# Kernel optimization log

Hardware: AMD Instinct MI355X
Metric: run time of the kernel (lower is better)

The kernel has to match this reference:

```python
import jax, jax.numpy as jnp
import numpy as np
from jax import lax

WIN = 9            # NCC_vxm default local window per dim
ITER_COUNT = 5
REG_WEIGHT = 1.0
LR, B1, B2, EPS = 0.1, 0.9, 0.999, 1e-8  # Adam(amsgrad=True) defaults + lr=0.1


def _window_sum(t, win=WIN):
    """Sum over a win^3 neighborhood (= conv3d with ones kernel, pad win//2),
    computed separably along each spatial axis. t: [B,1,H,W,D]."""
    pad = win // 2
    for ax in range(3):
        kshape = [1, 1, 1, 1, 1]
        kshape[2 + ax] = win
        k = jnp.ones(kshape, t.dtype)
        padding = [(pad, pad) if j == ax else (0, 0) for j in range(3)]
        t = lax.conv_general_dilated(t, k, (1, 1, 1), padding,
                                     dimension_numbers=('NCDHW', 'OIDHW', 'NCDHW'))
    return t


def ncc_loss(I, J):
    """voxelmorph local NCC (NCC_vxm), returns -mean(cc)."""
    win_size = float(WIN ** 3)
    I_sum = _window_sum(I)
    J_sum = _window_sum(J)
    I2_sum = _window_sum(I * I)
    J2_sum = _window_sum(J * J)
    IJ_sum = _window_sum(I * J)
    u_I = I_sum / win_size
    u_J = J_sum / win_size
    cross = IJ_sum - u_J * I_sum - u_I * J_sum + u_I * u_J * win_size
    I_var = I2_sum - 2.0 * u_I * I_sum + u_I * u_I * win_size
    J_var = J2_sum - 2.0 * u_J * J_sum + u_J * u_J * win_size
    cc = cross * cross / (I_var * J_var + 1e-5)
    return -jnp.mean(cc)


def grad3d_l2(flow):
    """Grad3d(penalty='l2'): mean squared finite differences, averaged over 3 axes."""
    dH = jnp.mean((flow[:, :, 1:] - flow[:, :, :-1]) ** 2)
    dW = jnp.mean((flow[:, :, :, 1:] - flow[:, :, :, :-1]) ** 2)
    dD = jnp.mean((flow[:, :, :, :, 1:] - flow[:, :, :, :, :-1]) ** 2)
    return (dH + dW + dD) / 3.0


def warp(x, flow):
    """SpatialTransformer: trilinear resample of x at (identity grid + flow),
    zero padding outside (torch grid_sample align_corners=True, padding 'zeros').
    x: [B,C,H,W,D], flow: [B,3,H,W,D]."""
    B, C, H, W, D = x.shape
    base = jnp.stack(jnp.meshgrid(jnp.arange(H, dtype=x.dtype),
                                  jnp.arange(W, dtype=x.dtype),
                                  jnp.arange(D, dtype=x.dtype),
                                  indexing='ij'), axis=0)          # [3,H,W,D]
    coords = base[None] + flow                                      # [B,3,H,W,D]

    def samp_one(vol, crd):  # vol [H,W,D], crd [3,H,W,D]
        return jax.scipy.ndimage.map_coordinates(
            vol, [crd[0], crd[1], crd[2]], order=1, mode='constant', cval=0.0)

    samp_batch = jax.vmap(lambda v, c: jax.vmap(lambda ch: samp_one(ch, c))(v))
    return samp_batch(x, coords)                                    # [B,C,H,W,D]


def _optimize_flow(x, y, initial_flow):
    """Inner OFG loop: 5 Adam(amsgrad) steps on the flow parameter."""
    def inner_loss(flow):
        x_warped = warp(x, flow)
        return ncc_loss(x_warped, y) + REG_WEIGHT * grad3d_l2(flow)

    grad_fn = jax.grad(inner_loss)
    flow = initial_flow
    m = jnp.zeros_like(flow)
    v = jnp.zeros_like(flow)
    vhat = jnp.zeros_like(flow)
    for t in range(1, ITER_COUNT + 1):
        g = grad_fn(flow)
        m = B1 * m + (1.0 - B1) * g
        v = B2 * v + (1.0 - B2) * g * g
        vhat = jnp.maximum(vhat, v)           # amsgrad
        m_hat = m / (1.0 - B1 ** t)
        denom = jnp.sqrt(vhat) / jnp.sqrt(1.0 - B2 ** t) + EPS
        flow = flow - LR * m_hat / denom
    return flow


def setup_inputs() -> dict:
    key = jax.random.key(0)
    k1, k2, k3 = jax.random.split(key, 3)
    H, W, D = 160, 192, 160
    x = jax.random.normal(k1, (1, 1, H, W, D), dtype=jnp.float32)
    y = jax.random.normal(k2, (1, 1, H, W, D), dtype=jnp.float32)
    initial_flow = jax.random.normal(k3, (1, 3, H, W, D), dtype=jnp.float32)
    return {"x": x, "y": y, "initial_flow": initial_flow}


def reference(x, y, initial_flow):
    flow = _optimize_flow(x, y, initial_flow)
    return jnp.mean((flow - initial_flow) ** 2)   # nn.MSELoss()
```

## Files before the change

kernel.cpp:

```cpp
#include <hip/hip_runtime.h>
#include <cmath>

#define HH 160
#define WW 192
#define DD 160
#define WD (WW*DD)
#define NPTS (HH*WW*DD)
#define NP4  (NPTS/4)
#define INV_WSZ (1.0f/729.0f)
#define ADAM_B1 0.9f
#define ADAM_B2 0.999f
#define ADAM_LR 0.1f
#define ADAM_EPS 1e-8f

__device__ __align__(16) float g_flowA[3*NPTS];
__device__ __align__(16) float g_flowB[3*NPTS];
__device__ __align__(16) float g_m   [3*NPTS];
__device__ __align__(16) float g_v   [3*NPTS];
__device__ __align__(16) float g_vh  [3*NPTS];
__device__ __align__(16) float g_X   [3*NPTS];
__device__ __align__(16) float g_Y   [3*NPTS];
__device__ __align__(16) float g_uJ  [NPTS];
__device__ __align__(16) float g_Jv  [NPTS];
__device__ double g_part[2048];


__device__ __forceinline__ float4 ld4(const float* p) { return *reinterpret_cast<const float4*>(p); }
__device__ __forceinline__ void  st4(float* p, float4 v) { *reinterpret_cast<float4*>(p) = v; }
#define UNPK(V,A) { A[0]=(V).x; A[1]=(V).y; A[2]=(V).z; A[3]=(V).w; }

__device__ __forceinline__ float fetchx(const float* __restrict__ x, int i, int j, int k) {
    if ((unsigned)i >= (unsigned)HH || (unsigned)j >= (unsigned)WW || (unsigned)k >= (unsigned)DD)
        return 0.0f;
    return x[(i*WW + j)*DD + k];
}

__device__ __forceinline__ void load12(const float* base, int idx, int dp, float* t) {
    float4 a = (dp == 0)    ? float4{0,0,0,0} : ld4(base + idx - 4);
    float4 b = ld4(base + idx);
    float4 c = (dp == DD-4) ? float4{0,0,0,0} : ld4(base + idx + 4);
    t[0]=a.x; t[1]=a.y; t[2]=a.z; t[3]=a.w;
    t[4]=b.x; t[5]=b.y; t[6]=b.z; t[7]=b.w;
    t[8]=c.x; t[9]=c.y; t[10]=c.z; t[11]=c.w;
}

__global__ void __launch_bounds__(320) warp_momD_k(
        const float* __restrict__ x, const float* __restrict__ y,
        const float* __restrict__ finit, int fin_code)
{
    __shared__ __align__(16) float sI[8][168];
    __shared__ __align__(16) float sJ[8][168];
    int tx = threadIdx.x;
    int ty = threadIdx.y;
    int line = blockIdx.x*8 + ty;
    int h = line / WW, w = line % WW;
    int dp = tx*4;
    int idx = line*DD + dp;
    const float* fin = (fin_code == 0) ? finit : ((fin_code == 1) ? g_flowA : g_flowB);

    float F0[4], F1[4], F2[4], Y4[4];
    { float4 a = ld4(fin + idx);          UNPK(a, F0); }
    { float4 a = ld4(fin + NPTS + idx);   UNPK(a, F1); }
    { float4 a = ld4(fin + 2*NPTS + idx); UNPK(a, F2); }
    { float4 a = ld4(y + idx);            UNPK(a, Y4); }

#pragma unroll
    for (int e = 0; e < 4; e++) {
        float c0 = (float)h + F0[e];
        float c1 = (float)w + F1[e];
        float c2 = (float)(dp + e) + F2[e];
        float fl0 = floorf(c0), fl1 = floorf(c1), fl2 = floorf(c2);
        int i0 = (int)fl0, j0 = (int)fl1, k0 = (int)fl2;
        float fx = c0 - fl0, fy = c1 - fl1, fz = c2 - fl2;
        float v000 = fetchx(x, i0,   j0,   k0  ), v001 = fetchx(x, i0,   j0,   k0+1);
        float v010 = fetchx(x, i0,   j0+1, k0  ), v011 = fetchx(x, i0,   j0+1, k0+1);
        float v100 = fetchx(x, i0+1, j0,   k0  ), v101 = fetchx(x, i0+1, j0,   k0+1);
        float v110 = fetchx(x, i0+1, j0+1, k0  ), v111 = fetchx(x, i0+1, j0+1, k0+1);
        float c00 = v000*(1.0f-fz) + v001*fz;
        float c01 = v010*(1.0f-fz) + v011*fz;
        float c10 = v100*(1.0f-fz) + v101*fz;
        float c11 = v110*(1.0f-fz) + v111*fz;
        float a0 = c00*(1.0f-fy) + c01*fy;
        float a1 = c10*(1.0f-fy) + c11*fy;
        sI[ty][4+dp+e] = a0*(1.0f-fx) + a1*fx;
        sJ[ty][4+dp+e] = Y4[e];
    }
    if (tx == 0) {
#pragma unroll
        for (int j = 0; j < 4; j++) { sI[ty][j] = 0.f; sJ[ty][j] = 0.f; }
    }
    if (tx == 39) {
#pragma unroll
        for (int j = 164; j < 168; j++) { sI[ty][j] = 0.f; sJ[ty][j] = 0.f; }
    }
    __syncthreads();

    float tI[12], tJ[12];
    { float4 a = ld4(&sI[ty][dp]);   UNPK(a, (&tI[0])); }
    { float4 a = ld4(&sI[ty][dp+4]); UNPK(a, (&tI[4])); }
    { float4 a = ld4(&sI[ty][dp+8]); UNPK(a, (&tI[8])); }
    { float4 a = ld4(&sJ[ty][dp]);   UNPK(a, (&tJ[0])); }
    { float4 a = ld4(&sJ[ty][dp+4]); UNPK(a, (&tJ[4])); }
    { float4 a = ld4(&sJ[ty][dp+8]); UNPK(a, (&tJ[8])); }

    float4 S1, S2, S3;
    float s1a[4], s2a[4], s3a[4];
#pragma unroll
    for (int e = 0; e < 4; e++) {
        float s1 = 0.f, s2 = 0.f, s3 = 0.f;
#pragma unroll
        for (int j = 0; j < 9; j++) {
            float a = tI[e+j], b = tJ[e+j];
            s1 += a; s2 += a*a; s3 += a*b;
        }
        s1a[e] = s1; s2a[e] = s2; s3a[e] = s3;
    }
    S1 = float4{s1a[0],s1a[1],s1a[2],s1a[3]};
    S2 = float4{s2a[0],s2a[1],s2a[2],s2a[3]};
    S3 = float4{s3a[0],s3a[1],s3a[2],s3a[3]};
    st4(g_X + idx, S1);
    st4(g_X + NPTS + idx, S2);
    st4(g_X + 2*NPTS + idx, S3);
}

template<int NF>
__global__ void __launch_bounds__(256) boxW_k()
{
    __shared__ __align__(16) float s[WW][32];
    int h  = blockIdx.x;
    int d0 = blockIdx.y*32;
    int t  = threadIdx.x;
#pragma unroll
    for (int f = 0; f < NF; f++) {
        const float* base = g_X + f*NPTS + h*WD + d0;
        for (int q = t; q < WW*8; q += 256) {
            int wq = q >> 3, dq = (q & 7)*4;
            st4(&s[wq][dq], ld4(base + wq*DD + dq));
        }
        __syncthreads();
        float* ob = g_Y + f*NPTS + h*WD + d0;
        for (int q = t; q < WW*8; q += 256) {
            int wq = q >> 3, dq = (q & 7)*4;
            int lo = (wq < 4) ? -wq : -4;
            int hi = (wq > WW-5) ? (WW-1-wq) : 4;
            float4 acc = float4{0,0,0,0};
            for (int k = lo; k <= hi; k++) {
                float4 v = ld4(&s[wq+k][dq]);
                acc.x += v.x; acc.y += v.y; acc.z += v.z; acc.w += v.w;
            }
            st4(ob + wq*DD + dq, acc);
        }
        __syncthreads();
    }
}

__global__ void __launch_bounds__(256) boxH_fields_k()
{
    __shared__ __align__(16) float sa[HH][16];
    __shared__ __align__(16) float sf[3][HH][16];
    int w  = blockIdx.x;
    int d0 = blockIdx.y*16;
    int t  = threadIdx.x;

#pragma unroll
    for (int f = 0; f < 3; f++) {
        const float* base = g_Y + f*NPTS + w*DD + d0;
        for (int q = t; q < HH*4; q += 256) {
            int hh = q >> 2, dq = (q & 3)*4;
            st4(&sa[hh][dq], ld4(base + hh*WD + dq));
        }
        __syncthreads();
        for (int q = t; q < HH*4; q += 256) {
            int hh = q >> 2, dq = (q & 3)*4;
            int lo = (hh < 4) ? -hh : -4;
            int hi = (hh > HH-5) ? (HH-1-hh) : 4;
            float4 acc = float4{0,0,0,0};
            for (int k = lo; k <= hi; k++) {
                float4 v = ld4(&sa[hh+k][dq]);
                acc.x += v.x; acc.y += v.y; acc.z += v.z; acc.w += v.w;
            }
            st4(&sf[f][hh][dq], acc);
        }
        __syncthreads();
    }

    for (int q = t; q < HH*4; q += 256) {
        int hh = q >> 2, dq = (q & 3)*4;
        int idxg = hh*WD + w*DD + d0 + dq;
        float Is[4], I2s[4], IJs[4], UJ[4], JV[4];
        { float4 a = ld4(&sf[0][hh][dq]); UNPK(a, Is); }
        { float4 a = ld4(&sf[1][hh][dq]); UNPK(a, I2s); }
        { float4 a = ld4(&sf[2][hh][dq]); UNPK(a, IJs); }
        { float4 a = ld4(g_uJ + idxg);    UNPK(a, UJ); }
        { float4 a = ld4(g_Jv + idxg);    UNPK(a, JV); }
        float A_[4], B_[4], C_[4];
#pragma unroll
        for (int e = 0; e < 4; e++) {
            float uI = Is[e] * INV_WSZ;
            float cross = IJs[e] - UJ[e]*Is[e];
            float Ivar  = I2s[e] - uI*Is[e];
            float den = Ivar*JV[e] + 1e-5f;
            float inv = 1.0f / den;
            float A = 2.0f*cross*inv;
            float B = -cross*cross*JV[e]*inv*inv;
            A_[e] = A; B_[e] = B; C_[e] = A*UJ[e] + 2.0f*B*uI;
        }
        st4(&sf[0][hh][dq], float4{A_[0],A_[1],A_[2],A_[3]});
        st4(&sf[1][hh][dq], float4{B_[0],B_[1],B_[2],B_[3]});
        st4(&sf[2][hh][dq], float4{C_[0],C_[1],C_[2],C_[3]});
    }
    __syncthreads();

#pragma unroll
    for (int f = 0; f < 3; f++) {
        float* ob = g_X + f*NPTS + w*DD + d0;
        for (int q = t; q < HH*4; q += 256) {
            int hh = q >> 2, dq = (q & 3)*4;
            int lo = (hh < 4) ? -hh : -4;
            int hi = (hh > HH-5) ? (HH-1-hh) : 4;
            float4 acc = float4{0,0,0,0};
            for (int k = lo; k <= hi; k++) {
                float4 v = ld4(&sf[f][hh+k][dq]);
                acc.x += v.x; acc.y += v.y; acc.z += v.z; acc.w += v.w;
            }
            st4(ob + hh*WD + dq, acc);
        }
    }
}


__global__ void __launch_bounds__(256) grad_adam_k(
        const float* __restrict__ x, const float* __restrict__ y,
        const float* __restrict__ finit,
        int fin_code, int fout_code,
        float inv_bc1, float inv_sqrt_bc2, int is_first)
{
    int p = blockIdx.x*blockDim.x + threadIdx.x;
    if (p >= NP4) return;
    int line = p / (DD/4);
    int dp   = (p % (DD/4))*4;
    int idx  = line*DD + dp;
    int w = line % WW;
    int h = line / WW;
    const float* fin = (fin_code == 0) ? finit : ((fin_code == 1) ? g_flowA : g_flowB);
    float* fout = (fout_code == 1) ? g_flowA : g_flowB;

    float SA[4], SB[4], SC[4];
    {
        float t[12];
        load12(g_Y,          idx, dp, t);
#pragma unroll
        for (int e = 0; e < 4; e++) { float s=0.f;
#pragma unroll
            for (int j = 0; j < 9; j++) s += t[e+j]; SA[e]=s; }
        load12(g_Y + NPTS,   idx, dp, t);
#pragma unroll
        for (int e = 0; e < 4; e++) { float s=0.f;
#pragma unroll
            for (int j = 0; j < 9; j++) s += t[e+j]; SB[e]=s; }
        load12(g_Y + 2*NPTS, idx, dp, t);
#pragma unroll
        for (int e = 0; e < 4; e++) { float s=0.f;
#pragma unroll
            for (int j = 0; j < 9; j++) s += t[e+j]; SC[e]=s; }
    }

    float F[3][4];
    { float4 a = ld4(fin + idx);          UNPK(a, F[0]); }
    { float4 a = ld4(fin + NPTS + idx);   UNPK(a, F[1]); }
    { float4 a = ld4(fin + 2*NPTS + idx); UNPK(a, F[2]); }
    float Y4[4];
    { float4 a = ld4(y + idx);            UNPK(a, Y4); }

    float GS[3][4];
#pragma unroll
    for (int e = 0; e < 4; e++) {
        int d = dp + e;
        float c0 = (float)h + F[0][e], c1 = (float)w + F[1][e], c2 = (float)d + F[2][e];
        float fl0 = floorf(c0), fl1 = floorf(c1), fl2 = floorf(c2);
        int i0 = (int)fl0, j0 = (int)fl1, k0 = (int)fl2;
        float fx = c0 - fl0, fy = c1 - fl1, fz = c2 - fl2;
        float v000 = fetchx(x, i0,   j0,   k0  ), v001 = fetchx(x, i0,   j0,   k0+1);
        float v010 = fetchx(x, i0,   j0+1, k0  ), v011 = fetchx(x, i0,   j0+1, k0+1);
        float v100 = fetchx(x, i0+1, j0,   k0  ), v101 = fetchx(x, i0+1, j0,   k0+1);
        float v110 = fetchx(x, i0+1, j0+1, k0  ), v111 = fetchx(x, i0+1, j0+1, k0+1);

        float c00 = v000*(1.0f-fz) + v001*fz;
        float c01 = v010*(1.0f-fz) + v011*fz;
        float c10 = v100*(1.0f-fz) + v101*fz;
        float c11 = v110*(1.0f-fz) + v111*fz;
        float a0 = c00*(1.0f-fy) + c01*fy;
        float a1 = c10*(1.0f-fy) + c11*fy;
        float Ival = a0*(1.0f-fx) + a1*fx;

        float gI = -(1.0f/(float)NPTS) * (Y4[e]*SA[e] + 2.0f*Ival*SB[e] - SC[e]);

        float gx = (1.0f-fy)*((v100-v000)*(1.0f-fz) + (v101-v001)*fz)
                 +        fy*((v110-v010)*(1.0f-fz) + (v111-v011)*fz);
        float gy = (1.0f-fx)*((v010-v000)*(1.0f-fz) + (v011-v001)*fz)
                 +        fx*((v110-v100)*(1.0f-fz) + (v111-v101)*fz);
        float gz = (1.0f-fx)*((v001-v000)*(1.0f-fy) + (v011-v010)*fy)
                 +        fx*((v101-v100)*(1.0f-fy) + (v111-v110)*fy);
        GS[0][e] = gI*gx; GS[1][e] = gI*gy; GS[2][e] = gI*gz;
    }

    const float coefH = 2.0f / (3.0f * (float)(3*(HH-1)*WW*DD));
    const float coefW = 2.0f / (3.0f * (float)(3*HH*(WW-1)*DD));
    const float coefD = 2.0f / (3.0f * (float)(3*HH*WW*(DD-1)));

#pragma unroll
    for (int c = 0; c < 3; c++) {
        const float* fc = fin + c*NPTS;
        int o = c*NPTS + idx;
        float FU[4], FD[4], FL[4], FR[4];
        { float4 a = (h > 0)    ? ld4(fc + idx - WD) : float4{0,0,0,0}; UNPK(a, FU); }
        { float4 a = (h < HH-1) ? ld4(fc + idx + WD) : float4{0,0,0,0}; UNPK(a, FD); }
        { float4 a = (w > 0)    ? ld4(fc + idx - DD) : float4{0,0,0,0}; UNPK(a, FL); }
        { float4 a = (w < WW-1) ? ld4(fc + idx + DD) : float4{0,0,0,0}; UNPK(a, FR); }
        float dl = (dp > 0)     ? fc[idx - 1] : 0.f;
        float dr = (dp < DD-4)  ? fc[idx + 4] : 0.f;

        float M[4], V[4], VH[4];
        if (is_first) {
#pragma unroll
            for (int e = 0; e < 4; e++) { M[e]=0.f; V[e]=0.f; VH[e]=0.f; }
        } else {
            { float4 a = ld4(g_m  + o); UNPK(a, M); }
            { float4 a = ld4(g_v  + o); UNPK(a, V); }
            { float4 a = ld4(g_vh + o); UNPK(a, VH); }
        }

        float O[4];
#pragma unroll
        for (int e = 0; e < 4; e++) {
            int d = dp + e;
            float f0 = F[c][e];
            float r = 0.0f;
            if (h > 0)     r += coefH*(f0 - FU[e]);
            if (h < HH-1)  r -= coefH*(FD[e] - f0);
            if (w > 0)     r += coefW*(f0 - FL[e]);
            if (w < WW-1)  r -= coefW*(FR[e] - f0);
            float left  = (e == 0) ? dl : F[c][e-1];
            float right = (e == 3) ? dr : F[c][e+1];
            if (d > 0)     r += coefD*(f0 - left);
            if (d < DD-1)  r -= coefD*(right - f0);
            float g = GS[c][e] + r;

            float mm  = ADAM_B1*M[e]  + (1.0f - ADAM_B1)*g;
            float vv  = ADAM_B2*V[e]  + (1.0f - ADAM_B2)*g*g;
            float vhh = fmaxf(VH[e], vv);
            M[e] = mm; V[e] = vv; VH[e] = vhh;
            float den = sqrtf(vhh)*inv_sqrt_bc2 + ADAM_EPS;
            O[e] = f0 - ADAM_LR*(mm*inv_bc1)/den;
        }
        st4(g_m  + o, float4{M[0],M[1],M[2],M[3]});
        st4(g_v  + o, float4{V[0],V[1],V[2],V[3]});
        st4(g_vh + o, float4{VH[0],VH[1],VH[2],VH[3]});
        st4(fout + o, float4{O[0],O[1],O[2],O[3]});
    }
}


__global__ void jmomD_k(const float* __restrict__ J)
{
    __shared__ float sJ[2][DD];
    int tx = threadIdx.x, ty = threadIdx.y;
    int line = blockIdx.x*2 + ty;
    int idx = line*DD + tx;
    sJ[ty][tx] = J[idx];
    __syncthreads();
    int lo = (tx < 4) ? -tx : -4;
    int hi = (tx > DD-5) ? (DD-1-tx) : 4;
    float s1 = 0.f, s2 = 0.f;
    for (int k = lo; k <= hi; k++) {
        float b = sJ[ty][tx+k];
        s1 += b; s2 += b*b;
    }
    g_X[idx] = s1; g_X[NPTS + idx] = s2;
}

__global__ void __launch_bounds__(256) boxH2_jstats_k()
{
    int p = blockIdx.x*blockDim.x + threadIdx.x;
    if (p >= NP4) return;
    int idx = p*4;
    int h = idx / WD;
    int lo = (h < 4) ? -h : -4;
    int hi = (h > HH-5) ? (HH-1-h) : 4;
    float4 s1 = float4{0,0,0,0}, s2 = float4{0,0,0,0};
    for (int k = lo; k <= hi; k++) {
        float4 a = ld4(g_Y + idx + k*WD);
        float4 b = ld4(g_Y + NPTS + idx + k*WD);
        s1.x += a.x; s1.y += a.y; s1.z += a.z; s1.w += a.w;
        s2.x += b.x; s2.y += b.y; s2.z += b.z; s2.w += b.w;
    }
    float4 u  = float4{s1.x*INV_WSZ, s1.y*INV_WSZ, s1.z*INV_WSZ, s1.w*INV_WSZ};
    float4 jv = float4{s2.x - u.x*s1.x, s2.y - u.y*s1.y, s2.z - u.z*s1.z, s2.w - u.w*s1.w};
    st4(g_uJ + idx, u);
    st4(g_Jv + idx, jv);
}


__global__ void mse_partial_k(const float* __restrict__ b)
{
    __shared__ double sd[256];
    int tid = threadIdx.x;
    double s = 0.0;
    for (int i = blockIdx.x*256 + tid; i < 3*NP4; i += gridDim.x*256) {
        float4 av = ld4(g_flowA + i*4);
        float4 bv = ld4(b + i*4);
        float d0 = av.x-bv.x, d1 = av.y-bv.y, d2 = av.z-bv.z, d3 = av.w-bv.w;
        s += (double)d0*(double)d0 + (double)d1*(double)d1
           + (double)d2*(double)d2 + (double)d3*(double)d3;
    }
    sd[tid] = s; __syncthreads();
    for (int o = 128; o > 0; o >>= 1) {
        if (tid < o) sd[tid] += sd[tid + o];
        __syncthreads();
    }
    if (tid == 0) g_part[blockIdx.x] = sd[0];
}

__global__ void mse_final_k(int nblk, float* __restrict__ out)
{
    __shared__ double sd[256];
    int tid = threadIdx.x;
    double s = 0.0;
    for (int i = tid; i < nblk; i += 256) s += g_part[i];
    sd[tid] = s; __syncthreads();
    for (int o = 128; o > 0; o >>= 1) {
        if (tid < o) sd[tid] += sd[tid + o];
        __syncthreads();
    }
    if (tid == 0) out[0] = (float)(sd[0] / (3.0*(double)NPTS));
}


extern "C" void kernel_launch(void* const* d_in, const int* in_sizes, int n_in,
                              void* d_out, int out_size, void* d_ws, size_t ws_size,
                              hipStream_t stream)
{
    const float* x    = (const float*)d_in[0];
    const float* y    = (const float*)d_in[1];
    const float* finit= (const float*)d_in[2];
    (void)d_ws; (void)ws_size;

    const int NB = 2048;
    dim3 blk(256);
    dim3 grd4((NP4 + 255)/256);
    dim3 lineBlk(DD, 2);
    dim3 lineGrd(HH*WW/2);
    dim3 wBlk(256);
    dim3 wGrd(HH, DD/32);
    dim3 hGrd(WW, DD/16);
    dim3 wmBlk(40, 8);
    dim3 wmGrd(HH*WW/8);

    jmomD_k<<<lineGrd, lineBlk, 0, stream>>>(y);
    boxW_k<2><<<wGrd, wBlk, 0, stream>>>();
    boxH2_jstats_k<<<grd4, blk, 0, stream>>>();

    int fin_code = 0, fout_code = 1;
    for (int t = 1; t <= 5; t++) {
        warp_momD_k<<<wmGrd, wmBlk, 0, stream>>>(x, y, finit, fin_code);
        boxW_k<3><<<wGrd, wBlk, 0, stream>>>();
        boxH_fields_k<<<hGrd, blk, 0, stream>>>();
        boxW_k<3><<<wGrd, wBlk, 0, stream>>>();
        double bc1 = 1.0 - pow(0.9, (double)t);
        double bc2 = 1.0 - pow(0.999, (double)t);
        grad_adam_k<<<grd4, blk, 0, stream>>>(x, y, finit, fin_code, fout_code,
                                              (float)(1.0/bc1), (float)(1.0/sqrt(bc2)),
                                              (t == 1) ? 1 : 0);
        fin_code = fout_code;
        fout_code = (fout_code == 1) ? 2 : 1;
    }

    mse_partial_k<<<NB, blk, 0, stream>>>(finit);
    mse_final_k<<<1, blk, 0, stream>>>(NB, (float*)d_out);
}
```

Baseline: 2.025 ms.

## Cache warped image and its spatial gradients instead of resampling in gradient kernel

The warp kernel now writes the trilinear-sampled intensity and the three interpolation gradients to new global buffers. The gradient/Adam kernel reads them instead of redoing the 8-point gather and interpolation from x. This removes a second random-access gather pass per iteration, at the cost of 4 extra NPTS-sized writes and reads. Separately, the H-axis box-filter kernel tile is halved in depth (16 to 8), doubling its grid to raise parallelism.

Result: faster. 1.867 ms (-7.8%).

```diff
diff --git a/kernel.cpp b/kernel.cpp
--- a/kernel.cpp
+++ b/kernel.cpp
@@ -20,6 +20,8 @@
 __device__ __align__(16) float g_vh  [3*NPTS];
 __device__ __align__(16) float g_X   [3*NPTS];
 __device__ __align__(16) float g_Y   [3*NPTS];
+__device__ __align__(16) float g_I   [NPTS];
+__device__ __align__(16) float g_G   [3*NPTS];
 __device__ __align__(16) float g_uJ  [NPTS];
 __device__ __align__(16) float g_Jv  [NPTS];
 __device__ double g_part[2048];
@@ -64,6 +66,7 @@
     { float4 a = ld4(fin + 2*NPTS + idx); UNPK(a, F2); }
     { float4 a = ld4(y + idx);            UNPK(a, Y4); }
 
+    float GX[4], GY[4], GZ[4], IV[4];
 #pragma unroll
     for (int e = 0; e < 4; e++) {
         float c0 = (float)h + F0[e];
@@ -82,9 +85,22 @@
         float c11 = v110*(1.0f-fz) + v111*fz;
         float a0 = c00*(1.0f-fy) + c01*fy;
         float a1 = c10*(1.0f-fy) + c11*fy;
-        sI[ty][4+dp+e] = a0*(1.0f-fx) + a1*fx;
+        float Ival = a0*(1.0f-fx) + a1*fx;
+        IV[e] = Ival;
+        sI[ty][4+dp+e] = Ival;
         sJ[ty][4+dp+e] = Y4[e];
-    }
+        GX[e] = (1.0f-fy)*((v100-v000)*(1.0f-fz) + (v101-v001)*fz)
+              +        fy*((v110-v010)*(1.0f-fz) + (v111-v011)*fz);
+        GY[e] = (1.0f-fx)*((v010-v000)*(1.0f-fz) + (v011-v001)*fz)
+              +        fx*((v110-v100)*(1.0f-fz) + (v111-v101)*fz);
+        GZ[e] = (1.0f-fx)*((v001-v000)*(1.0f-fy) + (v011-v010)*fy)
+              +        fx*((v101-v100)*(1.0f-fy) + (v111-v110)*fy);
+    }
+    st4(g_I + idx,          float4{IV[0],IV[1],IV[2],IV[3]});
+    st4(g_G + idx,          float4{GX[0],GX[1],GX[2],GX[3]});
+    st4(g_G + NPTS + idx,   float4{GY[0],GY[1],GY[2],GY[3]});
+    st4(g_G + 2*NPTS + idx, float4{GZ[0],GZ[1],GZ[2],GZ[3]});
+
     if (tx == 0) {
 #pragma unroll
         for (int j = 0; j < 4; j++) { sI[ty][j] = 0.f; sJ[ty][j] = 0.f; }
@@ -103,7 +119,6 @@
     { float4 a = ld4(&sJ[ty][dp+4]); UNPK(a, (&tJ[4])); }
     { float4 a = ld4(&sJ[ty][dp+8]); UNPK(a, (&tJ[8])); }
 
-    float4 S1, S2, S3;
     float s1a[4], s2a[4], s3a[4];
 #pragma unroll
     for (int e = 0; e < 4; e++) {
@@ -115,12 +130,9 @@
         }
         s1a[e] = s1; s2a[e] = s2; s3a[e] = s3;
     }
-    S1 = float4{s1a[0],s1a[1],s1a[2],s1a[3]};
-    S2 = float4{s2a[0],s2a[1],s2a[2],s2a[3]};
-    S3 = float4{s3a[0],s3a[1],s3a[2],s3a[3]};
-    st4(g_X + idx, S1);
-    st4(g_X + NPTS + idx, S2);
-    st4(g_X + 2*NPTS + idx, S3);
+    st4(g_X + idx,          float4{s1a[0],s1a[1],s1a[2],s1a[3]});
+    st4(g_X + NPTS + idx,   float4{s2a[0],s2a[1],s2a[2],s2a[3]});
+    st4(g_X + 2*NPTS + idx, float4{s3a[0],s3a[1],s3a[2],s3a[3]});
 }
 
 template<int NF>
@@ -156,22 +168,22 @@
 
 __global__ void __launch_bounds__(256) boxH_fields_k()
 {
-    __shared__ __align__(16) float sa[HH][16];
-    __shared__ __align__(16) float sf[3][HH][16];
+    __shared__ __align__(16) float sa[HH][8];
+    __shared__ __align__(16) float sf[3][HH][8];
     int w  = blockIdx.x;
-    int d0 = blockIdx.y*16;
+    int d0 = blockIdx.y*8;
     int t  = threadIdx.x;
 
 #pragma unroll
     for (int f = 0; f < 3; f++) {
         const float* base = g_Y + f*NPTS + w*DD + d0;
-        for (int q = t; q < HH*4; q += 256) {
-            int hh = q >> 2, dq = (q & 3)*4;
+        for (int q = t; q < HH*2; q += 256) {
+            int hh = q >> 1, dq = (q & 1)*4;
             st4(&sa[hh][dq], ld4(base + hh*WD + dq));
         }
         __syncthreads();
-        for (int q = t; q < HH*4; q += 256) {
-            int hh = q >> 2, dq = (q & 3)*4;
+        for (int q = t; q < HH*2; q += 256) {
+            int hh = q >> 1, dq = (q & 1)*4;
             int lo = (hh < 4) ? -hh : -4;
             int hi = (hh > HH-5) ? (HH-1-hh) : 4;
             float4 acc = float4{0,0,0,0};
@@ -184,8 +196,8 @@
         __syncthreads();
     }
 
-    for (int q = t; q < HH*4; q += 256) {
-        int hh = q >> 2, dq = (q & 3)*4;
+    for (int q = t; q < HH*2; q += 256) {
+        int hh = q >> 1, dq = (q & 1)*4;
         int idxg = hh*WD + w*DD + d0 + dq;
         float Is[4], I2s[4], IJs[4], UJ[4], JV[4];
         { float4 a = ld4(&sf[0][hh][dq]); UNPK(a, Is); }
@@ -214,8 +226,8 @@
 #pragma unroll
     for (int f = 0; f < 3; f++) {
         float* ob = g_X + f*NPTS + w*DD + d0;
-        for (int q = t; q < HH*4; q += 256) {
-            int hh = q >> 2, dq = (q & 3)*4;
+        for (int q = t; q < HH*2; q += 256) {
+            int hh = q >> 1, dq = (q & 1)*4;
             int lo = (hh < 4) ? -hh : -4;
             int hi = (hh > HH-5) ? (HH-1-hh) : 4;
             float4 acc = float4{0,0,0,0};
@@ -228,9 +240,8 @@
     }
 }
 
-
 __global__ void __launch_bounds__(256) grad_adam_k(
-        const float* __restrict__ x, const float* __restrict__ y,
+        const float* __restrict__ y,
         const float* __restrict__ finit,
         int fin_code, int fout_code,
         float inv_bc1, float inv_sqrt_bc2, int is_first)
@@ -269,39 +280,18 @@
     { float4 a = ld4(fin + idx);          UNPK(a, F[0]); }
     { float4 a = ld4(fin + NPTS + idx);   UNPK(a, F[1]); }
     { float4 a = ld4(fin + 2*NPTS + idx); UNPK(a, F[2]); }
-    float Y4[4];
+    float Y4[4], I4[4], GX[4], GY[4], GZ[4];
     { float4 a = ld4(y + idx);            UNPK(a, Y4); }
+    { float4 a = ld4(g_I + idx);          UNPK(a, I4); }
+    { float4 a = ld4(g_G + idx);          UNPK(a, GX); }
+    { float4 a = ld4(g_G + NPTS + idx);   UNPK(a, GY); }
+    { float4 a = ld4(g_G + 2*NPTS + idx); UNPK(a, GZ); }
 
     float GS[3][4];
 #pragma unroll
     for (int e = 0; e < 4; e++) {
-        int d = dp + e;
-        float c0 = (float)h + F[0][e], c1 = (float)w + F[1][e], c2 = (float)d + F[2][e];
-        float fl0 = floorf(c0), fl1 = floorf(c1), fl2 = floorf(c2);
-        int i0 = (int)fl0, j0 = (int)fl1, k0 = (int)fl2;
-        float fx = c0 - fl0, fy = c1 - fl1, fz = c2 - fl2;
-        float v000 = fetchx(x, i0,   j0,   k0  ), v001 = fetchx(x, i0,   j0,   k0+1);
-        float v010 = fetchx(x, i0,   j0+1, k0  ), v011 = fetchx(x, i0,   j0+1, k0+1);
-        float v100 = fetchx(x, i0+1, j0,   k0  ), v101 = fetchx(x, i0+1, j0,   k0+1);
-        float v110 = fetchx(x, i0+1, j0+1, k0  ), v111 = fetchx(x, i0+1, j0+1, k0+1);
-
-        float c00 = v000*(1.0f-fz) + v001*fz;
-        float c01 = v010*(1.0f-fz) + v011*fz;
-        float c10 = v100*(1.0f-fz) + v101*fz;
-        float c11 = v110*(1.0f-fz) + v111*fz;
-        float a0 = c00*(1.0f-fy) + c01*fy;
-        float a1 = c10*(1.0f-fy) + c11*fy;
-        float Ival = a0*(1.0f-fx) + a1*fx;
-
-        float gI = -(1.0f/(float)NPTS) * (Y4[e]*SA[e] + 2.0f*Ival*SB[e] - SC[e]);
-
-        float gx = (1.0f-fy)*((v100-v000)*(1.0f-fz) + (v101-v001)*fz)
-                 +        fy*((v110-v010)*(1.0f-fz) + (v111-v011)*fz);
-        float gy = (1.0f-fx)*((v010-v000)*(1.0f-fz) + (v011-v001)*fz)
-                 +        fx*((v110-v100)*(1.0f-fz) + (v111-v101)*fz);
-        float gz = (1.0f-fx)*((v001-v000)*(1.0f-fy) + (v011-v010)*fy)
-                 +        fx*((v101-v100)*(1.0f-fy) + (v111-v110)*fy);
-        GS[0][e] = gI*gx; GS[1][e] = gI*gy; GS[2][e] = gI*gz;
+        float gI = -(1.0f/(float)NPTS) * (Y4[e]*SA[e] + 2.0f*I4[e]*SB[e] - SC[e]);
+        GS[0][e] = gI*GX[e]; GS[1][e] = gI*GY[e]; GS[2][e] = gI*GZ[e];
     }
 
     const float coefH = 2.0f / (3.0f * (float)(3*(HH-1)*WW*DD));
@@ -452,7 +442,7 @@
     dim3 lineGrd(HH*WW/2);
     dim3 wBlk(256);
     dim3 wGrd(HH, DD/32);
-    dim3 hGrd(WW, DD/16);
+    dim3 hGrd(WW, DD/8);
     dim3 wmBlk(40, 8);
     dim3 wmGrd(HH*WW/8);
 
@@ -468,7 +458,7 @@
         boxW_k<3><<<wGrd, wBlk, 0, stream>>>();
         double bc1 = 1.0 - pow(0.9, (double)t);
         double bc2 = 1.0 - pow(0.999, (double)t);
-        grad_adam_k<<<grd4, blk, 0, stream>>>(x, y, finit, fin_code, fout_code,
+        grad_adam_k<<<grd4, blk, 0, stream>>>(y, finit, fin_code, fout_code,
                                               (float)(1.0/bc1), (float)(1.0/sqrt(bc2)),
                                               (t == 1) ? 1 : 0);
         fin_code = fout_code;
```
